# Kernel tuning notes

Measured on AMD Instinct MI355X. Metric: run time of the kernel, lower is better.

## Reference

```python
import jax, jax.numpy as jnp
import numpy as np

B, S, HID = 4, 1024, 1024
H = 16
D = HID // H  # 64
SPARSITY = 0.9  # keep prob = 0.1


def setup_inputs() -> dict:
    key = jax.random.key(0)
    ks = jax.random.split(key, 11)
    sc = 1.0 / np.sqrt(HID)
    x = jax.random.normal(ks[0], (B, S, HID), dtype=jnp.float32)
    Wq = jax.random.normal(ks[1], (HID, HID), dtype=jnp.float32) * sc
    bq = jnp.zeros((HID,), dtype=jnp.float32)
    Wk = jax.random.normal(ks[2], (HID, HID), dtype=jnp.float32) * sc
    bk = jnp.zeros((HID,), dtype=jnp.float32)
    Wv = jax.random.normal(ks[3], (HID, HID), dtype=jnp.float32) * sc
    bv = jnp.zeros((HID,), dtype=jnp.float32)
    Wo = jax.random.normal(ks[4], (HID, HID), dtype=jnp.float32) * sc
    bo = jnp.zeros((HID,), dtype=jnp.float32)
    temperature = jnp.ones((H, 1, 1), dtype=jnp.float32)
    # training-mode random sparsity mask: rand > sparsity -> keep (True)
    sparse_mask = jax.random.uniform(ks[5], (B, H, S, S)) > SPARSITY
    return {"x": x, "Wq": Wq, "bq": bq, "Wk": Wk, "bk": bk, "Wv": Wv,
            "bv": bv, "Wo": Wo, "bo": bo, "temperature": temperature,
            "sparse_mask": sparse_mask}


def reference(x, Wq, bq, Wk, bk, Wv, bv, Wo, bo, temperature, sparse_mask):
    b, s, _ = x.shape
    def split_heads(t):
        return t.reshape(b, s, H, D).transpose(0, 2, 1, 3)  # [B,H,S,D]
    q = split_heads(x @ Wq + bq)
    k = split_heads(x @ Wk + bk)
    v = split_heads(x @ Wv + bv)
    scores = jnp.einsum('bhqd,bhkd->bhqk', q, k) / np.sqrt(D)
    scores = scores * temperature  # [H,1,1] broadcasts over [B,H,S,S]
    scores = jnp.where(sparse_mask, scores, -jnp.inf)
    attn = jax.nn.softmax(scores, axis=-1)
    out = jnp.einsum('bhqk,bhkd->bhqd', attn, v)
    out = out.transpose(0, 2, 1, 3).reshape(b, s, HID)
    return out @ Wo + bo
```

## Files before the change

kernel.cpp:

```cpp
#include <hip/hip_runtime.h>

typedef unsigned short u16;
typedef short short8 __attribute__((ext_vector_type(8)));
typedef float f32x4 __attribute__((ext_vector_type(4)));
typedef float float4v __attribute__((ext_vector_type(4)));
typedef u16 u16x4 __attribute__((ext_vector_type(4)));
typedef unsigned uint2v __attribute__((ext_vector_type(2)));
typedef unsigned long long u64;

__device__ __forceinline__ u16 f2bf(float f) {
  union { float f; unsigned u; } v; v.f = f;
  unsigned r = v.u + 0x7FFFu + ((v.u >> 16) & 1u);
  return (u16)(r >> 16);
}

__device__ __forceinline__ unsigned cvtpk(float lo, float hi) {
  unsigned r;
  asm("v_cvt_pk_bf16_f32 %0, %1, %2" : "=v"(r) : "v"(lo), "v"(hi));
  return r;
}

__device__ __forceinline__ void gload16(const u16* g, u16* l) {
  __builtin_amdgcn_global_load_lds(
      (const __attribute__((address_space(1))) void*)g,
      (__attribute__((address_space(3))) void*)l, 16, 0, 0);
}

union PackSS { unsigned u[4]; short8 s; };

__global__ __launch_bounds__(256)
void prep_kernel(const void* __restrict__ mask, u64* __restrict__ bits,
                 const float* __restrict__ x, u16* __restrict__ xb,
                 const float* __restrict__ W0, const float* __restrict__ W1,
                 const float* __restrict__ W2, const float* __restrict__ W3,
                 u16* __restrict__ Wt) {
  __shared__ float t[32][33];
  __shared__ int sf;
  const int bid = blockIdx.x;
  if (bid < 4096) {
    if (threadIdx.x == 0) sf = 0;
    __syncthreads();
    {
      uint4 v = ((const uint4*)mask)[threadIdx.x];
      unsigned xs[4] = {v.x, v.y, v.z, v.w};
      int f = 0;
#pragma unroll
      for (int d = 0; d < 4; ++d) {
        unsigned u = xs[d];
        if (u == 0x3F800000u) f |= 1;
        if (u & 0xFFFFFF00u) f |= 2;
        if ((d & 1) && u) f |= 4;
      }
      if (f) atomicOr(&sf, f);
    }
    __syncthreads();
    const int fl = sf;
    const int fmt = (fl & 1) ? 2 : ((fl & 2) ? 0 : ((fl & 4) ? 1 : 3));

    const int wi = bid * 256 + threadIdx.x;
    u64 b = 0;
    if (fmt == 0) {
      const uint4* mp = (const uint4*)mask + (size_t)wi * 4;
#pragma unroll
      for (int i = 0; i < 4; ++i) {
        uint4 v = mp[i];
        unsigned xw[4] = {v.x, v.y, v.z, v.w};
#pragma unroll
        for (int d = 0; d < 4; ++d)
#pragma unroll
          for (int by = 0; by < 4; ++by)
            if (xw[d] & (0xFFu << (by * 8))) b |= 1ULL << (i * 16 + d * 4 + by);
      }
    } else if (fmt != 3) {
      const uint4* mp = (const uint4*)mask + (size_t)wi * 16;
#pragma unroll
      for (int i = 0; i < 16; ++i) {
        uint4 v = mp[i];
        if (v.x) b |= 1ULL << (i * 4 + 0);
        if (v.y) b |= 1ULL << (i * 4 + 1);
        if (v.z) b |= 1ULL << (i * 4 + 2);
        if (v.w) b |= 1ULL << (i * 4 + 3);
      }
    } else {
      const uint4* mp = (const uint4*)mask + (size_t)wi * 32;
#pragma unroll
      for (int i = 0; i < 32; ++i) {
        uint4 v = mp[i];
        if (v.x | v.y) b |= 1ULL << (i * 2 + 0);
        if (v.z | v.w) b |= 1ULL << (i * 2 + 1);
      }
    }
    int bh = wi >> 14, q = (wi >> 4) & 1023, kt = wi & 15;
    bits[((size_t)bh * 16 + kt) * 1024 + q] = b;
  } else if (bid < 8192) {
    int i = ((bid - 4096) * 256 + threadIdx.x) * 4;
    float4v v = *(const float4v*)(x + i);
    u16x4 o;
    o[0] = f2bf(v[0]); o[1] = f2bf(v[1]); o[2] = f2bf(v[2]); o[3] = f2bf(v[3]);
    *(u16x4*)(xb + i) = o;
  } else {
    int i = bid - 8192;
    int z = i >> 10, rest = i & 1023;
    const float* W = (z == 0) ? W0 : (z == 1) ? W1 : (z == 2) ? W2 : W3;
    u16* out = Wt + (size_t)z * 1024 * 1024;
    int n0 = (rest & 31) * 32, k0 = (rest >> 5) * 32;
    int tx = threadIdx.x & 31, ty = threadIdx.x >> 5;
#pragma unroll
    for (int j = 0; j < 4; ++j)
      t[ty + 8 * j][tx] = W[(size_t)(k0 + ty + 8 * j) * 1024 + n0 + tx];
    __syncthreads();
#pragma unroll
    for (int j = 0; j < 4; ++j)
      out[(size_t)(n0 + ty + 8 * j) * 1024 + k0 + tx] = f2bf(t[tx][ty + 8 * j]);
  }
}

template<int BN>
__global__ __launch_bounds__(256)
void gemm_kernel(const u16* __restrict__ A,
                 const u16* __restrict__ Bt0, const u16* __restrict__ Bt1, const u16* __restrict__ Bt2,
                 const float* __restrict__ b0, const float* __restrict__ b1, const float* __restrict__ b2,
                 const float* __restrict__ temp,
                 u16* __restrict__ qb, u16* __restrict__ kb, u16* __restrict__ vT,
                 float* __restrict__ fo, int phase) {
  constexpr int K = 1024;
  constexpr int WN = BN / 2;
  constexpr int NC = WN / 16;
  __shared__ u16 As[128 * 32];
  __shared__ u16 Bs[BN * 32];
  const int tid = threadIdx.x;
  const int lane = tid & 63, w = tid >> 6;
  const int l15 = lane & 15, l4 = lane >> 4;
  const int m0 = blockIdx.x * 128, n0 = blockIdx.y * BN;
  const int z = blockIdx.z;
  const u16* Bt = (z == 0) ? Bt0 : (z == 1) ? Bt1 : Bt2;
  const float* bias = (z == 0) ? b0 : (z == 1) ? b1 : b2;
  const int wr = w >> 1, wc = w & 1;

  f32x4 acc[4][NC] = {};

  const int c0 = tid, c1 = 256 + tid;
  const u16* ga0 = A + (size_t)(m0 + (c0 >> 2)) * K + (c0 & 3) * 8;
  const u16* ga1 = A + (size_t)(m0 + (c1 >> 2)) * K + (c1 & 3) * 8;
  const u16* gb0 = Bt + (size_t)(n0 + (c0 >> 2)) * K + (c0 & 3) * 8;
  const u16* gb1 = Bt + (size_t)(n0 + (c1 >> 2)) * K + (c1 & 3) * 8;
  u16* la0 = As + c0 * 8;
  u16* la1 = As + c1 * 8;
  u16* lb0 = Bs + c0 * 8;
  u16* lb1 = Bs + c1 * 8;

  for (int kt = 0; kt < K; kt += 32) {
    gload16(ga0 + kt, la0);
    gload16(ga1 + kt, la1);
    gload16(gb0 + kt, lb0);
    if (BN == 128) gload16(gb1 + kt, lb1);
    __syncthreads();
    short8 af[4], bfr[NC];
#pragma unroll
    for (int r = 0; r < 4; ++r)
      af[r] = *(const short8*)(As + (wr * 64 + r * 16 + l15) * 32 + l4 * 8);
#pragma unroll
    for (int c = 0; c < NC; ++c)
      bfr[c] = *(const short8*)(Bs + (wc * WN + c * 16 + l15) * 32 + l4 * 8);
#pragma unroll
    for (int r = 0; r < 4; ++r)
#pragma unroll
      for (int c = 0; c < NC; ++c)
        acc[r][c] = __builtin_amdgcn_mfma_f32_16x16x32_bf16(bfr[c], af[r], acc[r][c], 0, 0, 0);
    __syncthreads();
  }

  float bvj[NC][4];
#pragma unroll
  for (int c = 0; c < NC; ++c)
#pragma unroll
    for (int j = 0; j < 4; ++j)
      bvj[c][j] = bias[n0 + wc * WN + c * 16 + l4 * 4 + j];
  const float fac = (phase == 0 && z == 0)
      ? temp[(n0 + wc * WN) >> 6] * 0.18033688011112042f : 1.0f;

#pragma unroll
  for (int r = 0; r < 4; ++r) {
    const int mm = m0 + wr * 64 + r * 16 + l15;
    const int b = mm >> 10, s = mm & 1023;
#pragma unroll
    for (int c = 0; c < NC; ++c) {
      const int n = n0 + wc * WN + c * 16 + l4 * 4;
      if (phase == 1) {
        float4v o;
#pragma unroll
        for (int j = 0; j < 4; ++j) o[j] = acc[r][c][j] + bvj[c][j];
        *(float4v*)(fo + (size_t)mm * 1024 + n) = o;
      } else if (z == 2) {
#pragma unroll
        for (int j = 0; j < 4; ++j)
          vT[((size_t)b * 1024 + n + j) * 1024 + s] = f2bf(acc[r][c][j] + bvj[c][j]);
      } else {
        unsigned lo = cvtpk((acc[r][c][0] + bvj[c][0]) * fac, (acc[r][c][1] + bvj[c][1]) * fac);
        unsigned hi = cvtpk((acc[r][c][2] + bvj[c][2]) * fac, (acc[r][c][3] + bvj[c][3]) * fac);
        unsigned o2[2] = {lo, hi};
        int hh = n >> 6, d = n & 63;
        u16* dst = (z == 0) ? qb : kb;
        *(unsigned long long*)(dst + ((((size_t)b * 16 + hh) * 1024 + s) * 64 + d)) =
            *(unsigned long long*)o2;
      }
    }
  }
}

__global__ __launch_bounds__(512, 4)
void attn_kernel(const u16* __restrict__ qb, const u16* __restrict__ kb, const u16* __restrict__ vT,
                 const u64* __restrict__ mbits, u16* __restrict__ oh) {
  __shared__ u16 Ks[2][64 * 64];
  __shared__ u16 Vs[2][64 * 64];
  const int tid = threadIdx.x, lane = tid & 63, w = tid >> 6;
  const int l15 = lane & 15, l4 = lane >> 4;
  const int id = blockIdx.x;
  const int xcd = id & 7, sl = id >> 3;
  const int bh = xcd * 8 + (sl >> 3), qx = sl & 7;
  const int b = bh >> 4, h = bh & 15;
  const int q0 = qx * 128 + w * 16;
  const u16* qp = qb + ((size_t)bh * 1024 + q0) * 64;
  const u16* kp = kb + (size_t)bh * 1024 * 64;
  const u16* vp = vT + (size_t)bh * 64 * 1024;

  const int sr = tid >> 3, sc = ((tid & 7) ^ (sr & 7)) * 8;
  const int swz8 = (l15 & 7) << 3;
  const int vswz = l15 & 7;

  short8 qf0 = *(const short8*)(qp + (size_t)l15 * 64 + l4 * 8);
  short8 qf1 = *(const short8*)(qp + (size_t)l15 * 64 + 32 + l4 * 8);

  float m = -1e30f, l = 0.f;
  f32x4 oacc[4] = {};

  const u64* mb = mbits + (size_t)bh * 16 * 1024 + q0 + l15;
  u64 wcur = mb[0];

  gload16(kp + (size_t)sr * 64 + sc, &Ks[0][tid * 8]);
  gload16(vp + (size_t)sr * 1024 + sc, &Vs[0][tid * 8]);

  for (int t = 0; t < 16; ++t) {
    const int buf = t & 1;
    __syncthreads();

    if (t < 15) {
      const int k1 = (t + 1) * 64;
      gload16(kp + (size_t)(k1 + sr) * 64 + sc, &Ks[buf ^ 1][tid * 8]);
      gload16(vp + (size_t)sr * 1024 + k1 + sc, &Vs[buf ^ 1][tid * 8]);
    }
    u64 wnext = (t < 15) ? mb[(t + 1) * 1024] : 0ULL;

    f32x4 s[4] = {};
    __builtin_amdgcn_s_setprio(1);
#pragma unroll
    for (int cb = 0; cb < 4; ++cb) {
      const u16* kr = &Ks[buf][(cb * 16 + l15) * 64];
      short8 kf0 = *(const short8*)(kr + ((l4 * 8) ^ swz8));
      short8 kf1 = *(const short8*)(kr + ((32 + l4 * 8) ^ swz8));
      s[cb] = __builtin_amdgcn_mfma_f32_16x16x32_bf16(kf0, qf0, s[cb], 0, 0, 0);
      s[cb] = __builtin_amdgcn_mfma_f32_16x16x32_bf16(kf1, qf1, s[cb], 0, 0, 0);
    }
    __builtin_amdgcn_s_setprio(0);

    float mt = fmaxf(fmaxf(s[0][0], s[0][1]), fmaxf(s[0][2], s[0][3]));
#pragma unroll
    for (int cb = 1; cb < 4; ++cb)
      mt = fmaxf(mt, fmaxf(fmaxf(s[cb][0], s[cb][1]), fmaxf(s[cb][2], s[cb][3])));
    mt = fmaxf(mt, __shfl_xor(mt, 16));
    mt = fmaxf(mt, __shfl_xor(mt, 32));
    if (!__all(mt <= m + 8.f)) {
      float mnew = fmaxf(m, mt);
      float al = exp2f(m - mnew);
      l *= al;
#pragma unroll
      for (int db = 0; db < 4; ++db) oacc[db] *= al;
      m = mnew;
    }
    unsigned hws[4] = {(unsigned)wcur, (unsigned)(wcur >> 16),
                       (unsigned)(wcur >> 32), (unsigned)(wcur >> 48)};
    float rs = 0.f;
#pragma unroll
    for (int cb = 0; cb < 4; ++cb) {
#pragma unroll
      for (int j = 0; j < 4; ++j) {
        float p = exp2f(s[cb][j] - m);
        p = ((hws[cb] >> (l4 * 4 + j)) & 1) ? p : 0.f;
        rs += p;
        s[cb][j] = p;
      }
    }
    rs += __shfl_xor(rs, 16);
    rs += __shfl_xor(rs, 32);
    l += rs;

    PackSS pb0, pb1;
    pb0.u[0] = cvtpk(s[0][0], s[0][1]); pb0.u[1] = cvtpk(s[0][2], s[0][3]);
    pb0.u[2] = cvtpk(s[1][0], s[1][1]); pb0.u[3] = cvtpk(s[1][2], s[1][3]);
    pb1.u[0] = cvtpk(s[2][0], s[2][1]); pb1.u[1] = cvtpk(s[2][2], s[2][3]);
    pb1.u[2] = cvtpk(s[3][0], s[3][1]); pb1.u[3] = cvtpk(s[3][2], s[3][3]);

    __builtin_amdgcn_s_setprio(1);
#pragma unroll
    for (int kg = 0; kg < 2; ++kg) {
#pragma unroll
      for (int db = 0; db < 4; ++db) {
        const u16* vrow = &Vs[buf][(db * 16 + l15) * 64];
        const int e0 = (((4 * kg + (l4 >> 1)) ^ vswz) << 3) + (l4 & 1) * 4;
        const int e1 = (((4 * kg + 2 + (l4 >> 1)) ^ vswz) << 3) + (l4 & 1) * 4;
        uint2v v0 = *(const uint2v*)(vrow + e0);
        uint2v v1 = *(const uint2v*)(vrow + e1);
        PackSS vf;
        vf.u[0] = v0[0]; vf.u[1] = v0[1]; vf.u[2] = v1[0]; vf.u[3] = v1[1];
        oacc[db] = __builtin_amdgcn_mfma_f32_16x16x32_bf16(
            vf.s, kg ? pb1.s : pb0.s, oacc[db], 0, 0, 0);
      }
    }
    __builtin_amdgcn_s_setprio(0);
    wcur = wnext;
  }

  float rl = 1.f / l;
  u16* orow = oh + ((size_t)b * 1024 + q0 + l15) * 1024 + h * 64;
#pragma unroll
  for (int db = 0; db < 4; ++db) {
    unsigned a0 = cvtpk(oacc[db][0] * rl, oacc[db][1] * rl);
    unsigned a1 = cvtpk(oacc[db][2] * rl, oacc[db][3] * rl);
    unsigned oA[2] = {a0, a1};
    *(unsigned long long*)(orow + db * 16 + l4 * 4) = *(unsigned long long*)oA;
  }
}

extern "C" void kernel_launch(void* const* d_in, const int* in_sizes, int n_in,
                              void* d_out, int out_size, void* d_ws, size_t ws_size,
                              hipStream_t stream) {
  const float* x = (const float*)d_in[0];
  const float* Wq = (const float*)d_in[1];
  const float* bq = (const float*)d_in[2];
  const float* Wk = (const float*)d_in[3];
  const float* bk = (const float*)d_in[4];
  const float* Wv = (const float*)d_in[5];
  const float* bv = (const float*)d_in[6];
  const float* Wo = (const float*)d_in[7];
  const float* bo = (const float*)d_in[8];
  const float* temp = (const float*)d_in[9];
  const void* mask = (const void*)d_in[10];

  char* ws = (char*)d_ws;
  u16* xb = (u16*)(ws + 256);
  u16* Wt = xb + (size_t)4 * 1024 * 1024;
  u16* qbuf = Wt + (size_t)4 * 1024 * 1024;
  u16* kbuf = qbuf + (size_t)4 * 1024 * 1024;
  u16* vTb = kbuf + (size_t)4 * 1024 * 1024;
  u64* mbits = (u64*)(vTb + (size_t)4 * 1024 * 1024);
  u16* oh = xb;

  prep_kernel<<<12288, 256, 0, stream>>>(mask, mbits, x, xb, Wq, Wk, Wv, Wo, Wt);
  gemm_kernel<128><<<dim3(32, 8, 3), 256, 0, stream>>>(
      xb, Wt, Wt + 1024 * 1024, Wt + 2 * 1024 * 1024,
      bq, bk, bv, temp, qbuf, kbuf, vTb, nullptr, 0);
  attn_kernel<<<512, 512, 0, stream>>>(qbuf, kbuf, vTb, mbits, oh);
  gemm_kernel<64><<<dim3(32, 16, 1), 256, 0, stream>>>(
      oh, Wt + 3 * 1024 * 1024, nullptr, nullptr,
      bo, nullptr, nullptr, temp, nullptr, nullptr, nullptr, (float*)d_out, 1);
}
```

Baseline: 188.4 us.

## Fuse all four stages into one cooperative persistent kernel with grid syncs

```diff
diff --git a/kernel.cpp b/kernel.cpp
--- a/kernel.cpp
+++ b/kernel.cpp
@@ -1,4 +1,7 @@
 #include <hip/hip_runtime.h>
+#include <hip/hip_cooperative_groups.h>
+
+namespace cg = cooperative_groups;
 
 typedef unsigned short u16;
 typedef short short8 __attribute__((ext_vector_type(8)));
@@ -28,170 +31,154 @@
 
 union PackSS { unsigned u[4]; short8 s; };
 
-__global__ __launch_bounds__(256)
-void prep_kernel(const void* __restrict__ mask, u64* __restrict__ bits,
-                 const float* __restrict__ x, u16* __restrict__ xb,
-                 const float* __restrict__ W0, const float* __restrict__ W1,
-                 const float* __restrict__ W2, const float* __restrict__ W3,
-                 u16* __restrict__ Wt) {
-  __shared__ float t[32][33];
+__device__ void phase_prep(char* sm, const void* mask, u64* __restrict__ bits,
+                           const float* __restrict__ x, u16* __restrict__ xb,
+                           const float* __restrict__ W0, const float* __restrict__ W1,
+                           const float* __restrict__ W2, const float* __restrict__ W3,
+                           u16* __restrict__ Wt, int bid, int nb) {
   __shared__ int sf;
-  const int bid = blockIdx.x;
-  if (bid < 4096) {
-    if (threadIdx.x == 0) sf = 0;
+  if (threadIdx.x == 0) sf = 0;
+  __syncthreads();
+  {
+    uint4 v = ((const uint4*)mask)[threadIdx.x];
+    unsigned xs[4] = {v.x, v.y, v.z, v.w};
+    int f = 0;
+#pragma unroll
+    for (int d = 0; d < 4; ++d) {
+      unsigned u = xs[d];
+      if (u == 0x3F800000u) f |= 1;
+      if (u & 0xFFFFFF00u) f |= 2;
+      if ((d & 1) && u) f |= 4;
+    }
+    if (f) atomicOr(&sf, f);
+  }
+  __syncthreads();
+  const int fl = sf;
+  const int fmt = (fl & 1) ? 2 : ((fl & 2) ? 0 : ((fl & 4) ? 1 : 3));
+  float (*t)[33] = (float (*)[33])sm;
+
+  for (int vb = bid; vb < 12288; vb += nb) {
+    if (vb < 4096) {
+      const int wi = vb * 256 + threadIdx.x;
+      u64 b = 0;
+      if (fmt == 0) {
+        const uint4* mp = (const uint4*)mask + (size_t)wi * 4;
+#pragma unroll
+        for (int i = 0; i < 4; ++i) {
+          uint4 v = mp[i];
+          unsigned xw[4] = {v.x, v.y, v.z, v.w};
+#pragma unroll
+          for (int d = 0; d < 4; ++d)
+#pragma unroll
+            for (int by = 0; by < 4; ++by)
+              if (xw[d] & (0xFFu << (by * 8))) b |= 1ULL << (i * 16 + d * 4 + by);
+        }
+      } else if (fmt != 3) {
+        const uint4* mp = (const uint4*)mask + (size_t)wi * 16;
+#pragma unroll
+        for (int i = 0; i < 16; ++i) {
+          uint4 v = mp[i];
+          if (v.x) b |= 1ULL << (i * 4 + 0);
+          if (v.y) b |= 1ULL << (i * 4 + 1);
+          if (v.z) b |= 1ULL << (i * 4 + 2);
+          if (v.w) b |= 1ULL << (i * 4 + 3);
+        }
+      } else {
+        const uint4* mp = (const uint4*)mask + (size_t)wi * 32;
+#pragma unroll
+        for (int i = 0; i < 32; ++i) {
+          uint4 v = mp[i];
+          if (v.x | v.y) b |= 1ULL << (i * 2 + 0);
+          if (v.z | v.w) b |= 1ULL << (i * 2 + 1);
+        }
+      }
+      int bh = wi >> 14, q = (wi >> 4) & 1023, kt = wi & 15;
+      bits[((size_t)bh * 16 + kt) * 1024 + q] = b;
+    } else if (vb < 8192) {
+      int i = ((vb - 4096) * 256 + threadIdx.x) * 4;
+      float4v v = *(const float4v*)(x + i);
+      u16x4 o;
+      o[0] = f2bf(v[0]); o[1] = f2bf(v[1]); o[2] = f2bf(v[2]); o[3] = f2bf(v[3]);
+      *(u16x4*)(xb + i) = o;
+    } else {
+      int i = vb - 8192;
+      int z = i >> 10, rest = i & 1023;
+      const float* W = (z == 0) ? W0 : (z == 1) ? W1 : (z == 2) ? W2 : W3;
+      u16* outw = Wt + (size_t)z * 1048576;
+      int n0 = (rest & 31) * 32, k0 = (rest >> 5) * 32;
+      int tx = threadIdx.x & 31, ty = threadIdx.x >> 5;
+      __syncthreads();
+#pragma unroll
+      for (int j = 0; j < 4; ++j)
+        t[ty + 8 * j][tx] = W[(size_t)(k0 + ty + 8 * j) * 1024 + n0 + tx];
+      __syncthreads();
+#pragma unroll
+      for (int j = 0; j < 4; ++j)
+        outw[(size_t)(n0 + ty + 8 * j) * 1024 + k0 + tx] = f2bf(t[tx][ty + 8 * j]);
+    }
+  }
+}
+
+__device__ void phase_qkv(char* sm, const u16* __restrict__ A, const u16* __restrict__ Wt,
+                          const float* __restrict__ b0, const float* __restrict__ b1,
+                          const float* __restrict__ b2, const float* __restrict__ temp,
+                          u16* __restrict__ qb, u16* __restrict__ kb, u16* __restrict__ vT,
+                          int job) {
+  u16* As = (u16*)sm;
+  u16* Bs = (u16*)(sm + 8192);
+  const int z = job >> 8, rest = job & 255;
+  const int m0 = (rest >> 3) * 128, n0 = (rest & 7) * 128;
+  const u16* Bt = Wt + (size_t)z * 1048576;
+  const float* bias = (z == 0) ? b0 : (z == 1) ? b1 : b2;
+  const int tid = threadIdx.x, lane = tid & 63, w = tid >> 6;
+  const int l15 = lane & 15, l4 = lane >> 4;
+  const int wr = w >> 1, wc = w & 1;
+
+  f32x4 acc[4][4] = {};
+
+  const int c0 = tid, c1 = 256 + tid;
+  const u16* ga0 = A + (size_t)(m0 + (c0 >> 2)) * 1024 + (c0 & 3) * 8;
+  const u16* ga1 = A + (size_t)(m0 + (c1 >> 2)) * 1024 + (c1 & 3) * 8;
+  const u16* gb0 = Bt + (size_t)(n0 + (c0 >> 2)) * 1024 + (c0 & 3) * 8;
+  const u16* gb1 = Bt + (size_t)(n0 + (c1 >> 2)) * 1024 + (c1 & 3) * 8;
+
+  for (int kt = 0; kt < 1024; kt += 32) {
+    gload16(ga0 + kt, As + c0 * 8);
+    gload16(ga1 + kt, As + c1 * 8);
+    gload16(gb0 + kt, Bs + c0 * 8);
+    gload16(gb1 + kt, Bs + c1 * 8);
     __syncthreads();
-    {
-      uint4 v = ((const uint4*)mask)[threadIdx.x];
-      unsigned xs[4] = {v.x, v.y, v.z, v.w};
-      int f = 0;
-#pragma unroll
-      for (int d = 0; d < 4; ++d) {
-        unsigned u = xs[d];
-        if (u == 0x3F800000u) f |= 1;
-        if (u & 0xFFFFFF00u) f |= 2;
-        if ((d & 1) && u) f |= 4;
-      }
-      if (f) atomicOr(&sf, f);
-    }
-    __syncthreads();
-    const int fl = sf;
-    const int fmt = (fl & 1) ? 2 : ((fl & 2) ? 0 : ((fl & 4) ? 1 : 3));
-
-    const int wi = bid * 256 + threadIdx.x;
-    u64 b = 0;
-    if (fmt == 0) {
-      const uint4* mp = (const uint4*)mask + (size_t)wi * 4;
-#pragma unroll
-      for (int i = 0; i < 4; ++i) {
-        uint4 v = mp[i];
-        unsigned xw[4] = {v.x, v.y, v.z, v.w};
-#pragma unroll
-        for (int d = 0; d < 4; ++d)
-#pragma unroll
-          for (int by = 0; by < 4; ++by)
-            if (xw[d] & (0xFFu << (by * 8))) b |= 1ULL << (i * 16 + d * 4 + by);
-      }
-    } else if (fmt != 3) {
-      const uint4* mp = (const uint4*)mask + (size_t)wi * 16;
-#pragma unroll
-      for (int i = 0; i < 16; ++i) {
-        uint4 v = mp[i];
-        if (v.x) b |= 1ULL << (i * 4 + 0);
-        if (v.y) b |= 1ULL << (i * 4 + 1);
-        if (v.z) b |= 1ULL << (i * 4 + 2);
-        if (v.w) b |= 1ULL << (i * 4 + 3);
-      }
-    } else {
-      const uint4* mp = (const uint4*)mask + (size_t)wi * 32;
-#pragma unroll
-      for (int i = 0; i < 32; ++i) {
-        uint4 v = mp[i];
-        if (v.x | v.y) b |= 1ULL << (i * 2 + 0);
-        if (v.z | v.w) b |= 1ULL << (i * 2 + 1);
-      }
-    }
-    int bh = wi >> 14, q = (wi >> 4) & 1023, kt = wi & 15;
-    bits[((size_t)bh * 16 + kt) * 1024 + q] = b;
-  } else if (bid < 8192) {
-    int i = ((bid - 4096) * 256 + threadIdx.x) * 4;
-    float4v v = *(const float4v*)(x + i);
-    u16x4 o;
-    o[0] = f2bf(v[0]); o[1] = f2bf(v[1]); o[2] = f2bf(v[2]); o[3] = f2bf(v[3]);
-    *(u16x4*)(xb + i) = o;
-  } else {
-    int i = bid - 8192;
-    int z = i >> 10, rest = i & 1023;
-    const float* W = (z == 0) ? W0 : (z == 1) ? W1 : (z == 2) ? W2 : W3;
-    u16* out = Wt + (size_t)z * 1024 * 1024;
-    int n0 = (rest & 31) * 32, k0 = (rest >> 5) * 32;
-    int tx = threadIdx.x & 31, ty = threadIdx.x >> 5;
-#pragma unroll
-    for (int j = 0; j < 4; ++j)
-      t[ty + 8 * j][tx] = W[(size_t)(k0 + ty + 8 * j) * 1024 + n0 + tx];
-    __syncthreads();
-#pragma unroll
-    for (int j = 0; j < 4; ++j)
-      out[(size_t)(n0 + ty + 8 * j) * 1024 + k0 + tx] = f2bf(t[tx][ty + 8 * j]);
-  }
-}
-
-template<int BN>
-__global__ __launch_bounds__(256)
-void gemm_kernel(const u16* __restrict__ A,
-                 const u16* __restrict__ Bt0, const u16* __restrict__ Bt1, const u16* __restrict__ Bt2,
-                 const float* __restrict__ b0, const float* __restrict__ b1, const float* __restrict__ b2,
-                 const float* __restrict__ temp,
-                 u16* __restrict__ qb, u16* __restrict__ kb, u16* __restrict__ vT,
-                 float* __restrict__ fo, int phase) {
-  constexpr int K = 1024;
-  constexpr int WN = BN / 2;
-  constexpr int NC = WN / 16;
-  __shared__ u16 As[128 * 32];
-  __shared__ u16 Bs[BN * 32];
-  const int tid = threadIdx.x;
-  const int lane = tid & 63, w = tid >> 6;
-  const int l15 = lane & 15, l4 = lane >> 4;
-  const int m0 = blockIdx.x * 128, n0 = blockIdx.y * BN;
-  const int z = blockIdx.z;
-  const u16* Bt = (z == 0) ? Bt0 : (z == 1) ? Bt1 : Bt2;
-  const float* bias = (z == 0) ? b0 : (z == 1) ? b1 : b2;
-  const int wr = w >> 1, wc = w & 1;
-
-  f32x4 acc[4][NC] = {};
-
-  const int c0 = tid, c1 = 256 + tid;
-  const u16* ga0 = A + (size_t)(m0 + (c0 >> 2)) * K + (c0 & 3) * 8;
-  const u16* ga1 = A + (size_t)(m0 + (c1 >> 2)) * K + (c1 & 3) * 8;
-  const u16* gb0 = Bt + (size_t)(n0 + (c0 >> 2)) * K + (c0 & 3) * 8;
-  const u16* gb1 = Bt + (size_t)(n0 + (c1 >> 2)) * K + (c1 & 3) * 8;
-  u16* la0 = As + c0 * 8;
-  u16* la1 = As + c1 * 8;
-  u16* lb0 = Bs + c0 * 8;
-  u16* lb1 = Bs + c1 * 8;
-
-  for (int kt = 0; kt < K; kt += 32) {
-    gload16(ga0 + kt, la0);
-    gload16(ga1 + kt, la1);
-    gload16(gb0 + kt, lb0);
-    if (BN == 128) gload16(gb1 + kt, lb1);
-    __syncthreads();
-    short8 af[4], bfr[NC];
+    short8 af[4], bfr[4];
 #pragma unroll
     for (int r = 0; r < 4; ++r)
       af[r] = *(const short8*)(As + (wr * 64 + r * 16 + l15) * 32 + l4 * 8);
 #pragma unroll
-    for (int c = 0; c < NC; ++c)
-      bfr[c] = *(const short8*)(Bs + (wc * WN + c * 16 + l15) * 32 + l4 * 8);
+    for (int c = 0; c < 4; ++c)
+      bfr[c] = *(const short8*)(Bs + (wc * 64 + c * 16 + l15) * 32 + l4 * 8);
 #pragma unroll
     for (int r = 0; r < 4; ++r)
 #pragma unroll
-      for (int c = 0; c < NC; ++c)
+      for (int c = 0; c < 4; ++c)
         acc[r][c] = __builtin_amdgcn_mfma_f32_16x16x32_bf16(bfr[c], af[r], acc[r][c], 0, 0, 0);
     __syncthreads();
   }
 
-  float bvj[NC][4];
-#pragma unroll
-  for (int c = 0; c < NC; ++c)
+  float bvj[4][4];
+#pragma unroll
+  for (int c = 0; c < 4; ++c)
 #pragma unroll
     for (int j = 0; j < 4; ++j)
-      bvj[c][j] = bias[n0 + wc * WN + c * 16 + l4 * 4 + j];
-  const float fac = (phase == 0 && z == 0)
-      ? temp[(n0 + wc * WN) >> 6] * 0.18033688011112042f : 1.0f;
+      bvj[c][j] = bias[n0 + wc * 64 + c * 16 + l4 * 4 + j];
+  const float fac = (z == 0) ? temp[(n0 + wc * 64) >> 6] * 0.18033688011112042f : 1.0f;
 
 #pragma unroll
   for (int r = 0; r < 4; ++r) {
     const int mm = m0 + wr * 64 + r * 16 + l15;
     const int b = mm >> 10, s = mm & 1023;
 #pragma unroll
-    for (int c = 0; c < NC; ++c) {
-      const int n = n0 + wc * WN + c * 16 + l4 * 4;
-      if (phase == 1) {
-        float4v o;
-#pragma unroll
-        for (int j = 0; j < 4; ++j) o[j] = acc[r][c][j] + bvj[c][j];
-        *(float4v*)(fo + (size_t)mm * 1024 + n) = o;
-      } else if (z == 2) {
+    for (int c = 0; c < 4; ++c) {
+      const int n = n0 + wc * 64 + c * 16 + l4 * 4;
+      if (z == 2) {
 #pragma unroll
         for (int j = 0; j < 4; ++j)
           vT[((size_t)b * 1024 + n + j) * 1024 + s] = f2bf(acc[r][c][j] + bvj[c][j]);
@@ -208,23 +195,24 @@
   }
 }
 
-__global__ __launch_bounds__(512, 4)
-void attn_kernel(const u16* __restrict__ qb, const u16* __restrict__ kb, const u16* __restrict__ vT,
-                 const u64* __restrict__ mbits, u16* __restrict__ oh) {
-  __shared__ u16 Ks[2][64 * 64];
-  __shared__ u16 Vs[2][64 * 64];
+__device__ void phase_attn(char* sm, const u16* __restrict__ qb, const u16* __restrict__ kb,
+                           const u16* __restrict__ vT, const u64* __restrict__ mbits,
+                           u16* __restrict__ oh, int job) {
+  u16* Ks = (u16*)sm;
+  u16* Vs = (u16*)(sm + 16384);
   const int tid = threadIdx.x, lane = tid & 63, w = tid >> 6;
   const int l15 = lane & 15, l4 = lane >> 4;
-  const int id = blockIdx.x;
-  const int xcd = id & 7, sl = id >> 3;
-  const int bh = xcd * 8 + (sl >> 3), qx = sl & 7;
+  const int xcd = job & 7, rest = job >> 3;
+  const int bh = xcd * 8 + (rest & 7), qx = rest >> 3;
   const int b = bh >> 4, h = bh & 15;
-  const int q0 = qx * 128 + w * 16;
+  const int q0 = qx * 64 + w * 16;
   const u16* qp = qb + ((size_t)bh * 1024 + q0) * 64;
   const u16* kp = kb + (size_t)bh * 1024 * 64;
   const u16* vp = vT + (size_t)bh * 64 * 1024;
 
-  const int sr = tid >> 3, sc = ((tid & 7) ^ (sr & 7)) * 8;
+  const int L0 = tid, L1 = tid + 256;
+  const int r0 = L0 >> 3, c0 = ((L0 & 7) ^ (r0 & 7)) * 8;
+  const int r1 = L1 >> 3, c1 = ((L1 & 7) ^ (r1 & 7)) * 8;
   const int swz8 = (l15 & 7) << 3;
   const int vswz = l15 & 7;
 
@@ -237,17 +225,22 @@
   const u64* mb = mbits + (size_t)bh * 16 * 1024 + q0 + l15;
   u64 wcur = mb[0];
 
-  gload16(kp + (size_t)sr * 64 + sc, &Ks[0][tid * 8]);
-  gload16(vp + (size_t)sr * 1024 + sc, &Vs[0][tid * 8]);
+  gload16(kp + (size_t)r0 * 64 + c0, Ks + L0 * 8);
+  gload16(kp + (size_t)r1 * 64 + c1, Ks + L1 * 8);
+  gload16(vp + (size_t)r0 * 1024 + c0, Vs + L0 * 8);
+  gload16(vp + (size_t)r1 * 1024 + c1, Vs + L1 * 8);
 
   for (int t = 0; t < 16; ++t) {
-    const int buf = t & 1;
+    const int base = (t & 1) * 4096;
+    const int nbase = 4096 - base;
     __syncthreads();
 
     if (t < 15) {
       const int k1 = (t + 1) * 64;
-      gload16(kp + (size_t)(k1 + sr) * 64 + sc, &Ks[buf ^ 1][tid * 8]);
-      gload16(vp + (size_t)sr * 1024 + k1 + sc, &Vs[buf ^ 1][tid * 8]);
+      gload16(kp + (size_t)(k1 + r0) * 64 + c0, Ks + nbase + L0 * 8);
+      gload16(kp + (size_t)(k1 + r1) * 64 + c1, Ks + nbase + L1 * 8);
+      gload16(vp + (size_t)r0 * 1024 + k1 + c0, Vs + nbase + L0 * 8);
+      gload16(vp + (size_t)r1 * 1024 + k1 + c1, Vs + nbase + L1 * 8);
     }
     u64 wnext = (t < 15) ? mb[(t + 1) * 1024] : 0ULL;
 
@@ -255,7 +248,7 @@
     __builtin_amdgcn_s_setprio(1);
 #pragma unroll
     for (int cb = 0; cb < 4; ++cb) {
-      const u16* kr = &Ks[buf][(cb * 16 + l15) * 64];
+      const u16* kr = Ks + base + (cb * 16 + l15) * 64;
       short8 kf0 = *(const short8*)(kr + ((l4 * 8) ^ swz8));
       short8 kf1 = *(const short8*)(kr + ((32 + l4 * 8) ^ swz8));
       s[cb] = __builtin_amdgcn_mfma_f32_16x16x32_bf16(kf0, qf0, s[cb], 0, 0, 0);
@@ -305,7 +298,7 @@
     for (int kg = 0; kg < 2; ++kg) {
 #pragma unroll
       for (int db = 0; db < 4; ++db) {
-        const u16* vrow = &Vs[buf][(db * 16 + l15) * 64];
+        const u16* vrow = Vs + base + (db * 16 + l15) * 64;
         const int e0 = (((4 * kg + (l4 >> 1)) ^ vswz) << 3) + (l4 & 1) * 4;
         const int e1 = (((4 * kg + 2 + (l4 >> 1)) ^ vswz) << 3) + (l4 & 1) * 4;
         uint2v v0 = *(const uint2v*)(vrow + e0);
@@ -329,6 +322,102 @@
     unsigned oA[2] = {a0, a1};
     *(unsigned long long*)(orow + db * 16 + l4 * 4) = *(unsigned long long*)oA;
   }
+}
+
+__device__ void phase_oproj(char* sm, const u16* __restrict__ A, const u16* __restrict__ Bt,
+                            const float* __restrict__ bias, float* __restrict__ fo, int job) {
+  u16* As = (u16*)sm;
+  u16* Bs = (u16*)(sm + 4096);
+  const int tid = threadIdx.x, lane = tid & 63, w = tid >> 6;
+  const int l15 = lane & 15, l4 = lane >> 4;
+  const int m0 = (job >> 4) * 64, n0 = (job & 15) * 64;
+  const int wr = w >> 1, wc = w & 1;
+
+  f32x4 acc[2][2] = {};
+
+  const int rA = tid >> 2, cA = (tid & 3) * 8;
+  const u16* ga = A + (size_t)(m0 + rA) * 1024 + cA;
+  const u16* gb = Bt + (size_t)(n0 + rA) * 1024 + cA;
+
+  for (int kt = 0; kt < 1024; kt += 32) {
+    gload16(ga + kt, As + tid * 8);
+    gload16(gb + kt, Bs + tid * 8);
+    __syncthreads();
+    short8 af[2], bfr[2];
+#pragma unroll
+    for (int r = 0; r < 2; ++r)
+      af[r] = *(const short8*)(As + (wr * 32 + r * 16 + l15) * 32 + l4 * 8);
+#pragma unroll
+    for (int c = 0; c < 2; ++c)
+      bfr[c] = *(const short8*)(Bs + (wc * 32 + c * 16 + l15) * 32 + l4 * 8);
+#pragma unroll
+    for (int r = 0; r < 2; ++r)
+#pragma unroll
+      for (int c = 0; c < 2; ++c)
+        acc[r][c] = __builtin_amdgcn_mfma_f32_16x16x32_bf16(bfr[c], af[r], acc[r][c], 0, 0, 0);
+    __syncthreads();
+  }
+
+  float bvj[2][4];
+#pragma unroll
+  for (int c = 0; c < 2; ++c)
+#pragma unroll
+    for (int j = 0; j < 4; ++j)
+      bvj[c][j] = bias[n0 + wc * 32 + c * 16 + l4 * 4 + j];
+
+#pragma unroll
+  for (int r = 0; r < 2; ++r) {
+    const int mm = m0 + wr * 32 + r * 16 + l15;
+#pragma unroll
+    for (int c = 0; c < 2; ++c) {
+      const int n = n0 + wc * 32 + c * 16 + l4 * 4;
+      float4v o;
+#pragma unroll
+      for (int j = 0; j < 4; ++j) o[j] = acc[r][c][j] + bvj[c][j];
+      *(float4v*)(fo + (size_t)mm * 1024 + n) = o;
+    }
+  }
+}
+
+__global__ __launch_bounds__(256, 4)
+void fused_kernel(const void* mask, u64* mbits, const float* x, u16* xb,
+                  const float* Wq, const float* Wk, const float* Wv, const float* Wo,
+                  u16* Wt, const float* bq, const float* bk, const float* bv,
+                  const float* bo, const float* temp,
+                  u16* qb, u16* kb, u16* vT, u16* oh, float* out) {
+  __shared__ __align__(16) char sm[32768];
+  cg::grid_group grid = cg::this_grid();
+  phase_prep(sm, mask, mbits, x, xb, Wq, Wk, Wv, Wo, Wt, blockIdx.x, gridDim.x);
+  grid.sync();
+  if (blockIdx.x < 768)
+    phase_qkv(sm, xb, Wt, bq, bk, bv, temp, qb, kb, vT, blockIdx.x);
+  grid.sync();
+  phase_attn(sm, qb, kb, vT, mbits, oh, blockIdx.x);
+  grid.sync();
+  phase_oproj(sm, oh, Wt + (size_t)3 * 1048576, bo, out, blockIdx.x);
+}
+
+__global__ __launch_bounds__(256, 4)
+void k_prep(const void* mask, u64* mbits, const float* x, u16* xb,
+            const float* Wq, const float* Wk, const float* Wv, const float* Wo, u16* Wt) {
+  __shared__ __align__(16) char sm[32768];
+  phase_prep(sm, mask, mbits, x, xb, Wq, Wk, Wv, Wo, Wt, blockIdx.x, gridDim.x);
+}
+__global__ __launch_bounds__(256, 4)
+void k_qkv(const u16* xb, const u16* Wt, const float* bq, const float* bk,
+           const float* bv, const float* temp, u16* qb, u16* kb, u16* vT) {
+  __shared__ __align__(16) char sm[32768];
+  phase_qkv(sm, xb, Wt, bq, bk, bv, temp, qb, kb, vT, blockIdx.x);
+}
+__global__ __launch_bounds__(256, 4)
+void k_attn(const u16* qb, const u16* kb, const u16* vT, const u64* mbits, u16* oh) {
+  __shared__ __align__(16) char sm[32768];
+  phase_attn(sm, qb, kb, vT, mbits, oh, blockIdx.x);
+}
+__global__ __launch_bounds__(256, 4)
+void k_oproj(const u16* oh, const u16* WtO, const float* bo, float* out) {
+  __shared__ __align__(16) char sm[32768];
+  phase_oproj(sm, oh, WtO, bo, out, blockIdx.x);
 }
 
 extern "C" void kernel_launch(void* const* d_in, const int* in_sizes, int n_in,
@@ -354,13 +443,19 @@
   u16* vTb = kbuf + (size_t)4 * 1024 * 1024;
   u64* mbits = (u64*)(vTb + (size_t)4 * 1024 * 1024);
   u16* oh = xb;
-
-  prep_kernel<<<12288, 256, 0, stream>>>(mask, mbits, x, xb, Wq, Wk, Wv, Wo, Wt);
-  gemm_kernel<128><<<dim3(32, 8, 3), 256, 0, stream>>>(
-      xb, Wt, Wt + 1024 * 1024, Wt + 2 * 1024 * 1024,
-      bq, bk, bv, temp, qbuf, kbuf, vTb, nullptr, 0);
-  attn_kernel<<<512, 512, 0, stream>>>(qbuf, kbuf, vTb, mbits, oh);
-  gemm_kernel<64><<<dim3(32, 16, 1), 256, 0, stream>>>(
-      oh, Wt + 3 * 1024 * 1024, nullptr, nullptr,
-      bo, nullptr, nullptr, temp, nullptr, nullptr, nullptr, (float*)d_out, 1);
-}
+  float* outp = (float*)d_out;
+
+  void* ka[] = {(void*)&mask, (void*)&mbits, (void*)&x, (void*)&xb,
+                (void*)&Wq, (void*)&Wk, (void*)&Wv, (void*)&Wo, (void*)&Wt,
+                (void*)&bq, (void*)&bk, (void*)&bv, (void*)&bo, (void*)&temp,
+                (void*)&qbuf, (void*)&kbuf, (void*)&vTb, (void*)&oh, (void*)&outp};
+  hipError_t e = hipLaunchCooperativeKernel((const void*)fused_kernel,
+                                            dim3(1024), dim3(256), ka, 0, stream);
+  if (e != hipSuccess) {
+    (void)hipGetLastError();
+    k_prep<<<1024, 256, 0, stream>>>(mask, mbits, x, xb, Wq, Wk, Wv, Wo, Wt);
+    k_qkv<<<768, 256, 0, stream>>>(xb, Wt, bq, bk, bv, temp, qbuf, kbuf, vTb);
+    k_attn<<<1024, 256, 0, stream>>>(qbuf, kbuf, vTb, mbits, oh);
+    k_oproj<<<1024, 256, 0, stream>>>(oh, Wt + (size_t)3 * 1048576, bo, outp);
+  }
+}
```

Result: slower. 648.5 us (+244.2%).

## Read byte mask directly in attention via LDS instead of prepacking bits

Applied to the files above, without the earlier changes.

```diff
diff --git a/kernel.cpp b/kernel.cpp
--- a/kernel.cpp
+++ b/kernel.cpp
@@ -20,7 +20,7 @@
   return r;
 }
 
-__device__ __forceinline__ void gload16(const u16* g, u16* l) {
+__device__ __forceinline__ void gload16(const void* g, void* l) {
   __builtin_amdgcn_global_load_lds(
       (const __attribute__((address_space(1))) void*)g,
       (__attribute__((address_space(3))) void*)l, 16, 0, 0);
@@ -28,81 +28,43 @@
 
 union PackSS { unsigned u[4]; short8 s; };
 
+__device__ __forceinline__ int detect_fmt(const void* mask, int* sf) {
+  if (threadIdx.x == 0) *sf = 0;
+  __syncthreads();
+  uint4 v = ((const uint4*)mask)[threadIdx.x];
+  unsigned xs[4] = {v.x, v.y, v.z, v.w};
+  int f = 0;
+#pragma unroll
+  for (int d = 0; d < 4; ++d) {
+    unsigned u = xs[d];
+    if (u == 0x3F800000u) f |= 1;
+    if (u & 0xFFFFFF00u) f |= 2;
+    if ((d & 1) && u) f |= 4;
+  }
+  if (f) atomicOr(sf, f);
+  __syncthreads();
+  const int fl = *sf;
+  return (fl & 1) ? 2 : ((fl & 2) ? 0 : ((fl & 4) ? 1 : 3));
+}
+
 __global__ __launch_bounds__(256)
-void prep_kernel(const void* __restrict__ mask, u64* __restrict__ bits,
-                 const float* __restrict__ x, u16* __restrict__ xb,
-                 const float* __restrict__ W0, const float* __restrict__ W1,
-                 const float* __restrict__ W2, const float* __restrict__ W3,
-                 u16* __restrict__ Wt) {
+void cvt_kernel(const float* __restrict__ x, u16* __restrict__ xb,
+                const float* __restrict__ W0, const float* __restrict__ W1,
+                const float* __restrict__ W2, const float* __restrict__ W3,
+                u16* __restrict__ Wt) {
   __shared__ float t[32][33];
-  __shared__ int sf;
   const int bid = blockIdx.x;
   if (bid < 4096) {
-    if (threadIdx.x == 0) sf = 0;
-    __syncthreads();
-    {
-      uint4 v = ((const uint4*)mask)[threadIdx.x];
-      unsigned xs[4] = {v.x, v.y, v.z, v.w};
-      int f = 0;
-#pragma unroll
-      for (int d = 0; d < 4; ++d) {
-        unsigned u = xs[d];
-        if (u == 0x3F800000u) f |= 1;
-        if (u & 0xFFFFFF00u) f |= 2;
-        if ((d & 1) && u) f |= 4;
-      }
-      if (f) atomicOr(&sf, f);
-    }
-    __syncthreads();
-    const int fl = sf;
-    const int fmt = (fl & 1) ? 2 : ((fl & 2) ? 0 : ((fl & 4) ? 1 : 3));
-
-    const int wi = bid * 256 + threadIdx.x;
-    u64 b = 0;
-    if (fmt == 0) {
-      const uint4* mp = (const uint4*)mask + (size_t)wi * 4;
-#pragma unroll
-      for (int i = 0; i < 4; ++i) {
-        uint4 v = mp[i];
-        unsigned xw[4] = {v.x, v.y, v.z, v.w};
-#pragma unroll
-        for (int d = 0; d < 4; ++d)
-#pragma unroll
-          for (int by = 0; by < 4; ++by)
-            if (xw[d] & (0xFFu << (by * 8))) b |= 1ULL << (i * 16 + d * 4 + by);
-      }
-    } else if (fmt != 3) {
-      const uint4* mp = (const uint4*)mask + (size_t)wi * 16;
-#pragma unroll
-      for (int i = 0; i < 16; ++i) {
-        uint4 v = mp[i];
-        if (v.x) b |= 1ULL << (i * 4 + 0);
-        if (v.y) b |= 1ULL << (i * 4 + 1);
-        if (v.z) b |= 1ULL << (i * 4 + 2);
-        if (v.w) b |= 1ULL << (i * 4 + 3);
-      }
-    } else {
-      const uint4* mp = (const uint4*)mask + (size_t)wi * 32;
-#pragma unroll
-      for (int i = 0; i < 32; ++i) {
-        uint4 v = mp[i];
-        if (v.x | v.y) b |= 1ULL << (i * 2 + 0);
-        if (v.z | v.w) b |= 1ULL << (i * 2 + 1);
-      }
-    }
-    int bh = wi >> 14, q = (wi >> 4) & 1023, kt = wi & 15;
-    bits[((size_t)bh * 16 + kt) * 1024 + q] = b;
-  } else if (bid < 8192) {
-    int i = ((bid - 4096) * 256 + threadIdx.x) * 4;
+    int i = (bid * 256 + threadIdx.x) * 4;
     float4v v = *(const float4v*)(x + i);
     u16x4 o;
     o[0] = f2bf(v[0]); o[1] = f2bf(v[1]); o[2] = f2bf(v[2]); o[3] = f2bf(v[3]);
     *(u16x4*)(xb + i) = o;
   } else {
-    int i = bid - 8192;
+    int i = bid - 4096;
     int z = i >> 10, rest = i & 1023;
     const float* W = (z == 0) ? W0 : (z == 1) ? W1 : (z == 2) ? W2 : W3;
-    u16* out = Wt + (size_t)z * 1024 * 1024;
+    u16* outw = Wt + (size_t)z * 1048576;
     int n0 = (rest & 31) * 32, k0 = (rest >> 5) * 32;
     int tx = threadIdx.x & 31, ty = threadIdx.x >> 5;
 #pragma unroll
@@ -111,8 +73,39 @@
     __syncthreads();
 #pragma unroll
     for (int j = 0; j < 4; ++j)
-      out[(size_t)(n0 + ty + 8 * j) * 1024 + k0 + tx] = f2bf(t[tx][ty + 8 * j]);
-  }
+      outw[(size_t)(n0 + ty + 8 * j) * 1024 + k0 + tx] = f2bf(t[tx][ty + 8 * j]);
+  }
+}
+
+__global__ __launch_bounds__(256)
+void maskbits_kernel(const void* __restrict__ mask, u64* __restrict__ bits) {
+  __shared__ int sf;
+  const int fmt = detect_fmt(mask, &sf);
+  if (fmt == 0) return;
+
+  const int wi = blockIdx.x * 256 + threadIdx.x;
+  const int bh = wi >> 14, kt = (wi >> 10) & 15, q = wi & 1023;
+  u64 b = 0;
+  if (fmt != 3) {
+    const uint4* mp = (const uint4*)mask + (((size_t)bh << 18) + (q << 8) + (kt << 4));
+#pragma unroll
+    for (int i = 0; i < 16; ++i) {
+      uint4 v = mp[i];
+      if (v.x) b |= 1ULL << (i * 4 + 0);
+      if (v.y) b |= 1ULL << (i * 4 + 1);
+      if (v.z) b |= 1ULL << (i * 4 + 2);
+      if (v.w) b |= 1ULL << (i * 4 + 3);
+    }
+  } else {
+    const uint4* mp = (const uint4*)mask + (((size_t)bh << 19) + (q << 9) + (kt << 5));
+#pragma unroll
+    for (int i = 0; i < 32; ++i) {
+      uint4 v = mp[i];
+      if (v.x | v.y) b |= 1ULL << (i * 2 + 0);
+      if (v.z | v.w) b |= 1ULL << (i * 2 + 1);
+    }
+  }
+  bits[((size_t)bh * 16 + kt) * 1024 + q] = b;
 }
 
 template<int BN>
@@ -208,25 +201,36 @@
   }
 }
 
-__global__ __launch_bounds__(512, 4)
-void attn_kernel(const u16* __restrict__ qb, const u16* __restrict__ kb, const u16* __restrict__ vT,
+__global__ __launch_bounds__(256, 4)
+void attn_kernel(const u16* __restrict__ qb, const u16* __restrict__ kb,
+                 const u16* __restrict__ vT, const void* __restrict__ mask,
                  const u64* __restrict__ mbits, u16* __restrict__ oh) {
   __shared__ u16 Ks[2][64 * 64];
   __shared__ u16 Vs[2][64 * 64];
+  __shared__ u16 Ms[2][32 * 64];
+  __shared__ int sf;
+  const int fmt = detect_fmt(mask, &sf);
+
   const int tid = threadIdx.x, lane = tid & 63, w = tid >> 6;
   const int l15 = lane & 15, l4 = lane >> 4;
   const int id = blockIdx.x;
-  const int xcd = id & 7, sl = id >> 3;
-  const int bh = xcd * 8 + (sl >> 3), qx = sl & 7;
+  const int xcd = id & 7, rest = id >> 3;
+  const int bh = xcd * 8 + (rest & 7), qx = rest >> 3;
   const int b = bh >> 4, h = bh & 15;
-  const int q0 = qx * 128 + w * 16;
+  const int q0b = qx * 64;
+  const int q0 = q0b + w * 16;
   const u16* qp = qb + ((size_t)bh * 1024 + q0) * 64;
   const u16* kp = kb + (size_t)bh * 1024 * 64;
   const u16* vp = vT + (size_t)bh * 64 * 1024;
-
-  const int sr = tid >> 3, sc = ((tid & 7) ^ (sr & 7)) * 8;
+  const unsigned char* maskb = (const unsigned char*)mask + ((size_t)bh << 20);
+
+  const int L0 = tid, L1 = tid + 256;
+  const int r0 = L0 >> 3, c0 = ((L0 & 7) ^ (r0 & 7)) * 8;
+  const int r1 = L1 >> 3, c1 = ((L1 & 7) ^ (r1 & 7)) * 8;
   const int swz8 = (l15 & 7) << 3;
   const int vswz = l15 & 7;
+  const int mrow = tid >> 2, mcol = ((tid & 3) ^ (mrow & 3)) * 16;
+  const int rowb = w * 16 + l15;
 
   short8 qf0 = *(const short8*)(qp + (size_t)l15 * 64 + l4 * 8);
   short8 qf1 = *(const short8*)(qp + (size_t)l15 * 64 + 32 + l4 * 8);
@@ -235,10 +239,15 @@
   f32x4 oacc[4] = {};
 
   const u64* mb = mbits + (size_t)bh * 16 * 1024 + q0 + l15;
-  u64 wcur = mb[0];
-
-  gload16(kp + (size_t)sr * 64 + sc, &Ks[0][tid * 8]);
-  gload16(vp + (size_t)sr * 1024 + sc, &Vs[0][tid * 8]);
+  u64 wcur = 0;
+  if (fmt != 0) wcur = mb[0];
+
+  gload16(kp + (size_t)r0 * 64 + c0, &Ks[0][L0 * 8]);
+  gload16(kp + (size_t)r1 * 64 + c1, &Ks[0][L1 * 8]);
+  gload16(vp + (size_t)r0 * 1024 + c0, &Vs[0][L0 * 8]);
+  gload16(vp + (size_t)r1 * 1024 + c1, &Vs[0][L1 * 8]);
+  if (fmt == 0)
+    gload16(maskb + (size_t)(q0b + mrow) * 1024 + mcol, (u16*)Ms[0] + tid * 8);
 
   for (int t = 0; t < 16; ++t) {
     const int buf = t & 1;
@@ -246,10 +255,15 @@
 
     if (t < 15) {
       const int k1 = (t + 1) * 64;
-      gload16(kp + (size_t)(k1 + sr) * 64 + sc, &Ks[buf ^ 1][tid * 8]);
-      gload16(vp + (size_t)sr * 1024 + k1 + sc, &Vs[buf ^ 1][tid * 8]);
-    }
-    u64 wnext = (t < 15) ? mb[(t + 1) * 1024] : 0ULL;
+      gload16(kp + (size_t)(k1 + r0) * 64 + c0, &Ks[buf ^ 1][L0 * 8]);
+      gload16(kp + (size_t)(k1 + r1) * 64 + c1, &Ks[buf ^ 1][L1 * 8]);
+      gload16(vp + (size_t)r0 * 1024 + k1 + c0, &Vs[buf ^ 1][L0 * 8]);
+      gload16(vp + (size_t)r1 * 1024 + k1 + c1, &Vs[buf ^ 1][L1 * 8]);
+      if (fmt == 0)
+        gload16(maskb + (size_t)(q0b + mrow) * 1024 + k1 + mcol, (u16*)Ms[buf ^ 1] + tid * 8);
+    }
+    u64 wnext = 0;
+    if (fmt != 0 && t < 15) wnext = mb[(t + 1) * 1024];
 
     f32x4 s[4] = {};
     __builtin_amdgcn_s_setprio(1);
@@ -262,6 +276,20 @@
       s[cb] = __builtin_amdgcn_mfma_f32_16x16x32_bf16(kf1, qf1, s[cb], 0, 0, 0);
     }
     __builtin_amdgcn_s_setprio(0);
+
+    unsigned msel[4];
+    if (fmt == 0) {
+      const char* mr = (const char*)Ms[buf] + rowb * 64;
+#pragma unroll
+      for (int cb = 0; cb < 4; ++cb)
+        msel[cb] = *(const unsigned*)(mr + ((cb ^ (rowb & 3)) << 4) + l4 * 4);
+    } else {
+#pragma unroll
+      for (int cb = 0; cb < 4; ++cb) {
+        unsigned nib = (unsigned)(wcur >> (cb * 16 + l4 * 4)) & 15u;
+        msel[cb] = (nib * 0x00204081u) & 0x01010101u;
+      }
+    }
 
     float mt = fmaxf(fmaxf(s[0][0], s[0][1]), fmaxf(s[0][2], s[0][3]));
 #pragma unroll
@@ -277,15 +305,13 @@
       for (int db = 0; db < 4; ++db) oacc[db] *= al;
       m = mnew;
     }
-    unsigned hws[4] = {(unsigned)wcur, (unsigned)(wcur >> 16),
-                       (unsigned)(wcur >> 32), (unsigned)(wcur >> 48)};
     float rs = 0.f;
 #pragma unroll
     for (int cb = 0; cb < 4; ++cb) {
 #pragma unroll
       for (int j = 0; j < 4; ++j) {
         float p = exp2f(s[cb][j] - m);
-        p = ((hws[cb] >> (l4 * 4 + j)) & 1) ? p : 0.f;
+        p = (msel[cb] & (0xFFu << (j * 8))) ? p : 0.f;
         rs += p;
         s[cb][j] = p;
       }
@@ -355,12 +381,13 @@
   u64* mbits = (u64*)(vTb + (size_t)4 * 1024 * 1024);
   u16* oh = xb;
 
-  prep_kernel<<<12288, 256, 0, stream>>>(mask, mbits, x, xb, Wq, Wk, Wv, Wo, Wt);
+  cvt_kernel<<<8192, 256, 0, stream>>>(x, xb, Wq, Wk, Wv, Wo, Wt);
+  maskbits_kernel<<<4096, 256, 0, stream>>>(mask, mbits);
   gemm_kernel<128><<<dim3(32, 8, 3), 256, 0, stream>>>(
-      xb, Wt, Wt + 1024 * 1024, Wt + 2 * 1024 * 1024,
+      xb, Wt, Wt + 1048576, Wt + 2 * 1048576,
       bq, bk, bv, temp, qbuf, kbuf, vTb, nullptr, 0);
-  attn_kernel<<<512, 512, 0, stream>>>(qbuf, kbuf, vTb, mbits, oh);
+  attn_kernel<<<1024, 256, 0, stream>>>(qbuf, kbuf, vTb, mask, mbits, oh);
   gemm_kernel<64><<<dim3(32, 16, 1), 256, 0, stream>>>(
-      oh, Wt + 3 * 1024 * 1024, nullptr, nullptr,
+      oh, Wt + 3 * 1048576, nullptr, nullptr,
       bo, nullptr, nullptr, temp, nullptr, nullptr, nullptr, (float*)d_out, 1);
 }
```

New measurement: 220.8 us. 17.2% more time.
